# Kernel optimization log

Hardware: AMD Instinct MI355X
Metric: run time of the kernel (lower is better)

## Reference

```python
import jax, jax.numpy as jnp
import numpy as np

INPUT_SIZE = 64
HIDDEN_SIZE = 256
NUM_CLASSES = 10
BATCH = 512
SEQ_LEN = 1024


def setup_inputs() -> dict:
    key = jax.random.key(0)
    ks = jax.random.split(key, 6)
    std = 1.0 / np.sqrt(HIDDEN_SIZE)
    x = jax.random.normal(ks[0], (BATCH, SEQ_LEN, INPUT_SIZE), dtype=jnp.float32)
    # GRUCell params (reset_parameters: uniform(-std, std))
    Wx = jax.random.uniform(ks[1], (3 * HIDDEN_SIZE, INPUT_SIZE), minval=-std, maxval=std, dtype=jnp.float32)
    Wh = jax.random.uniform(ks[2], (3 * HIDDEN_SIZE, HIDDEN_SIZE), minval=-std, maxval=std, dtype=jnp.float32)
    bias = jax.random.uniform(ks[3], (3 * HIDDEN_SIZE,), minval=-std, maxval=std, dtype=jnp.float32)
    # fc: Linear(hidden_size, num_classes), default torch init ~ uniform(-1/sqrt(H), 1/sqrt(H))
    fc_w = jax.random.uniform(ks[4], (NUM_CLASSES, HIDDEN_SIZE), minval=-std, maxval=std, dtype=jnp.float32)
    fc_b = jax.random.uniform(ks[5], (NUM_CLASSES,), minval=-std, maxval=std, dtype=jnp.float32)
    return {"x": x, "Wx": Wx, "Wh": Wh, "bias": bias, "fc_w": fc_w, "fc_b": fc_b}


def reference(x, Wx, Wh, bias, fc_w, fc_b):
    B, S, _ = x.shape
    H = Wh.shape[1]
    b_r, b_z, b_h = jnp.split(bias, 3)
    # Precompute input gates for all timesteps in one GEMM: [B, S, 3H]
    gate_x = jnp.einsum('bsi,gi->bsg', x, Wx)

    def step(h, gx_t):
        gate_h = h @ Wh.T  # [B, 3H]
        i_r, i_z, i_h = jnp.split(gx_t, 3, axis=1)
        h_r, h_z, h_h = jnp.split(gate_h, 3, axis=1)
        reset_gate = jax.nn.sigmoid(i_r + h_r + b_r)
        update_gate = jax.nn.sigmoid(i_z + h_z + b_z)
        new_gate = jnp.tanh(i_h + reset_gate * h_h + b_h)
        hy = new_gate + update_gate * (h - new_gate)
        return hy, None

    h0 = jnp.zeros((B, H), dtype=x.dtype)
    hT, _ = jax.lax.scan(step, h0, jnp.swapaxes(gate_x, 0, 1))  # scan over time
    logit = hT @ fc_w.T + fc_b
    return logit
```

## Files before the change

kernel.cpp:

```cpp
#include <hip/hip_runtime.h>


typedef short v8s __attribute__((ext_vector_type(8)));
typedef float f32x4 __attribute__((ext_vector_type(4)));

#define LOG2E 1.4426950408889634f

__device__ __forceinline__ unsigned short f2b(float f) {
    unsigned int u = __float_as_uint(f);
    u += 0x7FFFu + ((u >> 16) & 1u);
    return (unsigned short)(u >> 16);
}
__device__ __forceinline__ float b2f(unsigned short h) {
    return __uint_as_float(((unsigned int)h) << 16);
}
__device__ __forceinline__ v8s cvt8(f32x4 a, f32x4 b) {
    v8s r;
#pragma unroll
    for (int j = 0; j < 4; ++j) { r[j] = (short)f2b(a[j]); r[4 + j] = (short)f2b(b[j]); }
    return r;
}
__device__ __forceinline__ v8s wfrag(const float* src, float s) {
    f32x4 a = *(const f32x4*)src, b = *(const f32x4*)(src + 4);
    a *= s; b *= s;
    return cvt8(a, b);
}
__device__ __forceinline__ float rcpf(float v) {
#if __has_builtin(__builtin_amdgcn_rcpf)
    return __builtin_amdgcn_rcpf(v);
#else
    return 1.0f / v;
#endif
}
__device__ __forceinline__ float exp2f_(float v) {
#if __has_builtin(__builtin_amdgcn_exp2f)
    return __builtin_amdgcn_exp2f(v);
#else
    return __exp2f(v);
#endif
}
__device__ __forceinline__ float sg(float v) { return rcpf(1.0f + exp2f_(-v)); }
__device__ __forceinline__ f32x4 MF(v8s a, v8s b, f32x4 c) {
    return __builtin_amdgcn_mfma_f32_16x16x32_bf16(a, b, c, 0, 0, 0);
}
__device__ __forceinline__ int fidx(int row, int k) {
    return ((k >> 5) << 9) + ((((k >> 3) & 3) << 4) + row) * 8 + (k & 7);
}

#define LDS_H    131072
#define LDS_X    147456
#define LDS_SIZE 151552

extern "C" __global__ void __launch_bounds__(512, 2)
gru_v7(const float* __restrict__ x, const float* __restrict__ Wx,
       const float* __restrict__ Wh, const float* __restrict__ bias,
       const float* __restrict__ fcw, const float* __restrict__ fcb,
       float* __restrict__ out)
{
    extern __shared__ char lds[];
    v8s* whn = (v8s*)lds;
    char* hl = lds + LDS_H;
    char* xl = lds + LDS_X;

    const int tid = threadIdx.x;
    const int w = tid >> 6, l = tid & 63;
    const int cl = l & 15, kg = l >> 4;
    const int b0 = blockIdx.x << 4;
    const int tiles[6] = {2*w, 2*w+1, 16+2*w, 17+2*w, 32+2*w, 33+2*w};

    for (int f = w; f < 128; f += 8) {
        int t5 = f >> 3, ks = f & 7;
        const float* src = Wh + (size_t)(512 + t5*16 + cl)*256 + ks*32 + kg*8;
        whn[f*64 + l] = wfrag(src, 2.0f*LOG2E);
    }
    v8s whB[4][8];
#pragma unroll
    for (int tt = 0; tt < 4; ++tt) {
        const float* src = Wh + (size_t)(tiles[tt]*16 + cl)*256 + kg*8;
#pragma unroll
        for (int ks = 0; ks < 8; ++ks)
            whB[tt][ks] = wfrag(src + ks*32, LOG2E);
    }
    v8s wxr[12];
#pragma unroll
    for (int tt = 0; tt < 6; ++tt) {
        const float sc = (tt < 4) ? LOG2E : 2.0f*LOG2E;
        const float* s0 = Wx + (size_t)(tiles[tt]*16 + cl)*64 + kg*8;
        wxr[tt*2]   = wfrag(s0, sc);
        wxr[tt*2+1] = wfrag(s0 + 32, sc);
    }
    float brv[2], bzv[2], bhv[2];
#pragma unroll
    for (int p = 0; p < 2; ++p) {
        int ch = (w << 5) + (p << 4) + cl;
        brv[p] = bias[ch] * LOG2E;
        bzv[p] = bias[256 + ch] * LOG2E;
        bhv[p] = bias[512 + ch] * 2.0f*LOG2E;
    }

    for (int i = tid; i < 2048; i += 512) ((unsigned int*)hl)[i] = 0u;
    float hprev[8] = {0, 0, 0, 0, 0, 0, 0, 0};

    const int xr = tid >> 5, xc = (tid & 31) << 1;
    const int xidx = fidx(xr, xc);
    const float* xp = x + (((size_t)(b0 + xr)) << 16) + xc;
    {
        unsigned int pk = (unsigned int)f2b(xp[0]) | ((unsigned int)f2b(xp[1]) << 16);
        *(unsigned int*)(xl + xidx*2) = pk;
    }
    xp += 64;
    const int wn0 = (2*w)*8, wn1 = (2*w+1)*8;

    for (int t = 0; t < 1024; ++t) {
        __syncthreads();
        const int cur = t & 1;
        const v8s* hb = (const v8s*)(hl + cur*8192);
        const v8s* xb = (const v8s*)(xl + cur*2048);

        float xv0 = 0.0f, xv1 = 0.0f;
        if (t < 1023) { xv0 = xp[0]; xv1 = xp[1]; xp += 64; }

        f32x4 acc[8];
        acc[0] = f32x4{brv[0], brv[0], brv[0], brv[0]};
        acc[1] = f32x4{brv[1], brv[1], brv[1], brv[1]};
        acc[2] = f32x4{bzv[0], bzv[0], bzv[0], bzv[0]};
        acc[3] = f32x4{bzv[1], bzv[1], bzv[1], bzv[1]};
        acc[4] = f32x4{0, 0, 0, 0};
        acc[5] = f32x4{0, 0, 0, 0};
        acc[6] = f32x4{bhv[0], bhv[0], bhv[0], bhv[0]};
        acc[7] = f32x4{bhv[1], bhv[1], bhv[1], bhv[1]};

#pragma unroll
        for (int ks = 0; ks < 8; ++ks) {
            v8s a  = hb[(ks << 6) + l];
            v8s n0 = whn[(wn0 + ks)*64 + l];
            v8s n1 = whn[(wn1 + ks)*64 + l];
            acc[0] = MF(a, whB[0][ks], acc[0]);
            acc[1] = MF(a, whB[1][ks], acc[1]);
            acc[2] = MF(a, whB[2][ks], acc[2]);
            acc[3] = MF(a, whB[3][ks], acc[3]);
            acc[4] = MF(a, n0, acc[4]);
            acc[5] = MF(a, n1, acc[5]);
        }
#pragma unroll
        for (int k2 = 0; k2 < 2; ++k2) {
            v8s ax = xb[(k2 << 6) + l];
            acc[0] = MF(ax, wxr[0  + k2], acc[0]);
            acc[1] = MF(ax, wxr[2  + k2], acc[1]);
            acc[2] = MF(ax, wxr[4  + k2], acc[2]);
            acc[3] = MF(ax, wxr[6  + k2], acc[3]);
            acc[6] = MF(ax, wxr[8  + k2], acc[6]);
            acc[7] = MF(ax, wxr[10 + k2], acc[7]);
        }

        unsigned short* hn = (unsigned short*)(hl + (cur ^ 1) * 8192);
#pragma unroll
        for (int p = 0; p < 2; ++p) {
            const int ch = (w << 5) + (p << 4) + cl;
            const int chbase = ((ch >> 5) << 9) + (((ch >> 3) & 3) << 7) + (ch & 7);
#pragma unroll
            for (int i = 0; i < 4; ++i) {
                float rg = sg(acc[p][i]);
                float zg = sg(acc[2 + p][i]);
                float nv = __builtin_fmaf(rg, acc[4 + p][i], acc[6 + p][i]);
                float ng = __builtin_fmaf(2.0f, sg(nv), -1.0f);
                float hy = ng + zg * (hprev[p*4 + i] - ng);
                hprev[p*4 + i] = hy;
                hn[chbase + ((kg << 2) + i) * 8] = f2b(hy);
            }
        }
        if (t < 1023) {
            unsigned int pk = (unsigned int)f2b(xv0) | ((unsigned int)f2b(xv1) << 16);
            *(unsigned int*)(xl + ((cur ^ 1) * 2048) + xidx*2) = pk;
        }
    }

    __syncthreads();
    const unsigned short* hf = (const unsigned short*)hl;
    if (tid < 160) {
        int row = tid / 10, cls = tid - row * 10;
        float s = fcb[cls];
        const float* wrow = fcw + cls * 256;
        for (int k = 0; k < 256; ++k)
            s += b2f(hf[fidx(row, k)]) * wrow[k];
        out[(b0 + row)*10 + cls] = s;
    }
}

extern "C" void kernel_launch(void* const* d_in, const int* in_sizes, int n_in,
                              void* d_out, int out_size, void* d_ws, size_t ws_size,
                              hipStream_t stream) {
    const float* x    = (const float*)d_in[0];
    const float* Wx   = (const float*)d_in[1];
    const float* Wh   = (const float*)d_in[2];
    const float* bias = (const float*)d_in[3];
    const float* fcw  = (const float*)d_in[4];
    const float* fcb  = (const float*)d_in[5];
    (void)d_ws; (void)ws_size;

    (void)hipFuncSetAttribute((const void*)gru_v7,
                              hipFuncAttributeMaxDynamicSharedMemorySize, LDS_SIZE);
    gru_v7<<<dim3(32), dim3(512), LDS_SIZE, stream>>>(
        x, Wx, Wh, bias, fcw, fcb, (float*)d_out);
}
```

Measured before the change: 1.967 ms.

## Double threads per block so each wave owns one 16-channel tile per gate

Raises the block from 512 to 1024 threads (16 waves), so each wave computes one 16-channel tile per gate instead of two. This halves the per-wave MFMA chain and gate math on the serial recurrence critical path. Register-resident weight fragments per thread drop accordingly. In exchange the per-step __syncthreads spans twice as many waves, and each thread now loads one x value rather than two.

Measured after the change: 1.995 ms. No clear change (+1.4%).

```diff
diff --git a/kernel.cpp b/kernel.cpp
--- a/kernel.cpp
+++ b/kernel.cpp
@@ -47,132 +47,105 @@
     return ((k >> 5) << 9) + ((((k >> 3) & 3) << 4) + row) * 8 + (k & 7);
 }
 
-#define LDS_H    131072
-#define LDS_X    147456
-#define LDS_SIZE 151552
+#define LDSX_WN   0
+#define LDSX_H    131072
+#define LDSX_X    147456
+#define LDSX_SIZE 151552
 
-extern "C" __global__ void __launch_bounds__(512, 2)
-gru_v7(const float* __restrict__ x, const float* __restrict__ Wx,
-       const float* __restrict__ Wh, const float* __restrict__ bias,
-       const float* __restrict__ fcw, const float* __restrict__ fcb,
-       float* __restrict__ out)
+extern "C" __global__ void __launch_bounds__(1024, 4)
+gru_v10(const float* __restrict__ x, const float* __restrict__ Wx,
+        const float* __restrict__ Wh, const float* __restrict__ bias,
+        const float* __restrict__ fcw, const float* __restrict__ fcb,
+        float* __restrict__ out)
 {
     extern __shared__ char lds[];
-    v8s* whn = (v8s*)lds;
-    char* hl = lds + LDS_H;
-    char* xl = lds + LDS_X;
+    v8s* wnl = (v8s*)(lds + LDSX_WN);
+    char* hl = lds + LDSX_H;
+    char* xl = lds + LDSX_X;
 
     const int tid = threadIdx.x;
     const int w = tid >> 6, l = tid & 63;
     const int cl = l & 15, kg = l >> 4;
     const int b0 = blockIdx.x << 4;
-    const int tiles[6] = {2*w, 2*w+1, 16+2*w, 17+2*w, 32+2*w, 33+2*w};
+    const int ch = (w << 4) + cl;
 
-    for (int f = w; f < 128; f += 8) {
-        int t5 = f >> 3, ks = f & 7;
-        const float* src = Wh + (size_t)(512 + t5*16 + cl)*256 + ks*32 + kg*8;
-        whn[f*64 + l] = wfrag(src, 2.0f*LOG2E);
+#pragma unroll
+    for (int ks = 0; ks < 8; ++ks)
+        wnl[(w*8 + ks)*64 + l] =
+            wfrag(Wh + (size_t)(512 + ch)*256 + ks*32 + kg*8, 2.0f*LOG2E);
+
+    v8s rW[10], zW[10], nX[2];
+#pragma unroll
+    for (int ks = 0; ks < 8; ++ks) {
+        rW[ks] = wfrag(Wh + (size_t)ch*256 + ks*32 + kg*8, LOG2E);
+        zW[ks] = wfrag(Wh + (size_t)(256 + ch)*256 + ks*32 + kg*8, LOG2E);
     }
-    v8s whB[4][8];
 #pragma unroll
-    for (int tt = 0; tt < 4; ++tt) {
-        const float* src = Wh + (size_t)(tiles[tt]*16 + cl)*256 + kg*8;
-#pragma unroll
-        for (int ks = 0; ks < 8; ++ks)
-            whB[tt][ks] = wfrag(src + ks*32, LOG2E);
+    for (int k2 = 0; k2 < 2; ++k2) {
+        rW[8+k2] = wfrag(Wx + (size_t)ch*64 + k2*32 + kg*8, LOG2E);
+        zW[8+k2] = wfrag(Wx + (size_t)(256 + ch)*64 + k2*32 + kg*8, LOG2E);
+        nX[k2]   = wfrag(Wx + (size_t)(512 + ch)*64 + k2*32 + kg*8, 2.0f*LOG2E);
     }
-    v8s wxr[12];
-#pragma unroll
-    for (int tt = 0; tt < 6; ++tt) {
-        const float sc = (tt < 4) ? LOG2E : 2.0f*LOG2E;
-        const float* s0 = Wx + (size_t)(tiles[tt]*16 + cl)*64 + kg*8;
-        wxr[tt*2]   = wfrag(s0, sc);
-        wxr[tt*2+1] = wfrag(s0 + 32, sc);
+    const float br = bias[ch] * LOG2E;
+    const float bz = bias[256 + ch] * LOG2E;
+    const float bn = bias[512 + ch] * (2.0f*LOG2E);
+
+    const int chb = ((ch >> 5) << 9) + (((ch >> 3) & 3) << 7) + (ch & 7);
+
+    for (int i = tid; i < 2048; i += 1024) ((unsigned int*)hl)[i] = 0u;
+    float hprev[4] = {0, 0, 0, 0};
+
+    const int xr = tid >> 6, xc = tid & 63;
+    const int xidx = fidx(xr, xc);
+    {
+        float v = x[((size_t)(b0 + xr) * 1024 + 0) * 64 + xc];
+        *(unsigned short*)(xl + xidx*2) = f2b(v);
     }
-    float brv[2], bzv[2], bhv[2];
-#pragma unroll
-    for (int p = 0; p < 2; ++p) {
-        int ch = (w << 5) + (p << 4) + cl;
-        brv[p] = bias[ch] * LOG2E;
-        bzv[p] = bias[256 + ch] * LOG2E;
-        bhv[p] = bias[512 + ch] * 2.0f*LOG2E;
-    }
-
-    for (int i = tid; i < 2048; i += 512) ((unsigned int*)hl)[i] = 0u;
-    float hprev[8] = {0, 0, 0, 0, 0, 0, 0, 0};
-
-    const int xr = tid >> 5, xc = (tid & 31) << 1;
-    const int xidx = fidx(xr, xc);
-    const float* xp = x + (((size_t)(b0 + xr)) << 16) + xc;
-    {
-        unsigned int pk = (unsigned int)f2b(xp[0]) | ((unsigned int)f2b(xp[1]) << 16);
-        *(unsigned int*)(xl + xidx*2) = pk;
-    }
-    xp += 64;
-    const int wn0 = (2*w)*8, wn1 = (2*w+1)*8;
 
     for (int t = 0; t < 1024; ++t) {
         __syncthreads();
         const int cur = t & 1;
-        const v8s* hb = (const v8s*)(hl + cur*8192);
-        const v8s* xb = (const v8s*)(xl + cur*2048);
+        const v8s* hb = (const v8s*)(hl + cur * 8192);
+        const v8s* xb = (const v8s*)(xl + cur * 2048);
 
-        float xv0 = 0.0f, xv1 = 0.0f;
-        if (t < 1023) { xv0 = xp[0]; xv1 = xp[1]; xp += 64; }
+        float xv = 0.0f;
+        if (t < 1023)
+            xv = x[((size_t)(b0 + xr) * 1024 + (t + 1)) * 64 + xc];
 
-        f32x4 acc[8];
-        acc[0] = f32x4{brv[0], brv[0], brv[0], brv[0]};
-        acc[1] = f32x4{brv[1], brv[1], brv[1], brv[1]};
-        acc[2] = f32x4{bzv[0], bzv[0], bzv[0], bzv[0]};
-        acc[3] = f32x4{bzv[1], bzv[1], bzv[1], bzv[1]};
-        acc[4] = f32x4{0, 0, 0, 0};
-        acc[5] = f32x4{0, 0, 0, 0};
-        acc[6] = f32x4{bhv[0], bhv[0], bhv[0], bhv[0]};
-        acc[7] = f32x4{bhv[1], bhv[1], bhv[1], bhv[1]};
+        f32x4 aR = {br, br, br, br};
+        f32x4 aZ = {bz, bz, bz, bz};
+        f32x4 aNh = {0, 0, 0, 0};
+        f32x4 aNx = {bn, bn, bn, bn};
 
 #pragma unroll
         for (int ks = 0; ks < 8; ++ks) {
             v8s a  = hb[(ks << 6) + l];
-            v8s n0 = whn[(wn0 + ks)*64 + l];
-            v8s n1 = whn[(wn1 + ks)*64 + l];
-            acc[0] = MF(a, whB[0][ks], acc[0]);
-            acc[1] = MF(a, whB[1][ks], acc[1]);
-            acc[2] = MF(a, whB[2][ks], acc[2]);
-            acc[3] = MF(a, whB[3][ks], acc[3]);
-            acc[4] = MF(a, n0, acc[4]);
-            acc[5] = MF(a, n1, acc[5]);
+            v8s nW = wnl[(w*8 + ks)*64 + l];
+            aR  = MF(a, rW[ks], aR);
+            aZ  = MF(a, zW[ks], aZ);
+            aNh = MF(a, nW, aNh);
         }
 #pragma unroll
         for (int k2 = 0; k2 < 2; ++k2) {
             v8s ax = xb[(k2 << 6) + l];
-            acc[0] = MF(ax, wxr[0  + k2], acc[0]);
-            acc[1] = MF(ax, wxr[2  + k2], acc[1]);
-            acc[2] = MF(ax, wxr[4  + k2], acc[2]);
-            acc[3] = MF(ax, wxr[6  + k2], acc[3]);
-            acc[6] = MF(ax, wxr[8  + k2], acc[6]);
-            acc[7] = MF(ax, wxr[10 + k2], acc[7]);
+            aR  = MF(ax, rW[8+k2], aR);
+            aZ  = MF(ax, zW[8+k2], aZ);
+            aNx = MF(ax, nX[k2], aNx);
         }
 
         unsigned short* hn = (unsigned short*)(hl + (cur ^ 1) * 8192);
 #pragma unroll
-        for (int p = 0; p < 2; ++p) {
-            const int ch = (w << 5) + (p << 4) + cl;
-            const int chbase = ((ch >> 5) << 9) + (((ch >> 3) & 3) << 7) + (ch & 7);
-#pragma unroll
-            for (int i = 0; i < 4; ++i) {
-                float rg = sg(acc[p][i]);
-                float zg = sg(acc[2 + p][i]);
-                float nv = __builtin_fmaf(rg, acc[4 + p][i], acc[6 + p][i]);
-                float ng = __builtin_fmaf(2.0f, sg(nv), -1.0f);
-                float hy = ng + zg * (hprev[p*4 + i] - ng);
-                hprev[p*4 + i] = hy;
-                hn[chbase + ((kg << 2) + i) * 8] = f2b(hy);
-            }
+        for (int i = 0; i < 4; ++i) {
+            float rg = sg(aR[i]);
+            float zg = sg(aZ[i]);
+            float nv = __builtin_fmaf(rg, aNh[i], aNx[i]);
+            float ng = __builtin_fmaf(2.0f, sg(nv), -1.0f);
+            float hy = ng + zg * (hprev[i] - ng);
+            hprev[i] = hy;
+            hn[chb + ((kg << 2) + i) * 8] = f2b(hy);
         }
-        if (t < 1023) {
-            unsigned int pk = (unsigned int)f2b(xv0) | ((unsigned int)f2b(xv1) << 16);
-            *(unsigned int*)(xl + ((cur ^ 1) * 2048) + xidx*2) = pk;
-        }
+        if (t < 1023)
+            *(unsigned short*)(xl + (cur ^ 1) * 2048 + xidx*2) = f2b(xv);
     }
 
     __syncthreads();
@@ -183,7 +156,7 @@
         const float* wrow = fcw + cls * 256;
         for (int k = 0; k < 256; ++k)
             s += b2f(hf[fidx(row, k)]) * wrow[k];
-        out[(b0 + row)*10 + cls] = s;
+        out[(b0 + row) * 10 + cls] = s;
     }
 }
 
@@ -198,8 +171,8 @@
     const float* fcb  = (const float*)d_in[5];
     (void)d_ws; (void)ws_size;
 
-    (void)hipFuncSetAttribute((const void*)gru_v7,
-                              hipFuncAttributeMaxDynamicSharedMemorySize, LDS_SIZE);
-    gru_v7<<<dim3(32), dim3(512), LDS_SIZE, stream>>>(
+    (void)hipFuncSetAttribute((const void*)gru_v10,
+                              hipFuncAttributeMaxDynamicSharedMemorySize, LDSX_SIZE);
+    gru_v10<<<dim3(32), dim3(1024), LDSX_SIZE, stream>>>(
         x, Wx, Wh, bias, fcw, fcb, (float*)d_out);
 }
```

## Split input-gate GEMM into producer blocks streaming fp16 gates via workspace ring

Applied to the files above, without the earlier changes.

Adds a persistent kernel in which 224 producer blocks compute the input-projection gates (x·Wx + bias) in chunks, write them to a global workspace ring buffer as fp16, and signal per-chunk completion through atomic counters. The 32 recurrent blocks spin-wait on these counters and read precomputed gates, so their per-step work is reduced to the h·Wh MFMAs. All of Wh, including the n-gate weights previously held in LDS, now lives in registers, which shrinks the LDS footprint. The design relies on all 256 blocks being co-resident for the spin-wait handshake to make progress, adds global-memory traffic for the gate tensor, and introduces fp16 rounding of the input gates. The old kernel is kept as a fallback when the workspace is too small.

Result: slower. 3.451 ms (+75.5%).

```diff
diff --git a/kernel.cpp b/kernel.cpp
--- a/kernel.cpp
+++ b/kernel.cpp
@@ -1,8 +1,10 @@
 #include <hip/hip_runtime.h>
+#include <hip/hip_fp16.h>
 
 
 typedef short v8s __attribute__((ext_vector_type(8)));
 typedef float f32x4 __attribute__((ext_vector_type(4)));
+typedef unsigned int u32x4 __attribute__((ext_vector_type(4)));
 
 #define LOG2E 1.4426950408889634f
 
@@ -13,6 +15,13 @@
 }
 __device__ __forceinline__ float b2f(unsigned short h) {
     return __uint_as_float(((unsigned int)h) << 16);
+}
+__device__ __forceinline__ unsigned short f2h(float f) {
+    return __half_as_ushort(__float2half_rn(f));
+}
+__device__ __forceinline__ float hxu(unsigned int u, int hi) {
+    unsigned short b = (unsigned short)(hi ? (u >> 16) : (u & 0xFFFFu));
+    return __half2float(__ushort_as_half(b));
 }
 __device__ __forceinline__ v8s cvt8(f32x4 a, f32x4 b) {
     v8s r;
@@ -47,9 +56,197 @@
     return ((k >> 5) << 9) + ((((k >> 3) & 3) << 4) + row) * 8 + (k & 7);
 }
 
-#define LDS_H    131072
-#define LDS_X    147456
-#define LDS_SIZE 151552
+#define LDS11_SIZE 98304
+
+extern "C" __global__ void __launch_bounds__(512, 2)
+gru_v11(const float* __restrict__ x, const float* __restrict__ Wx,
+        const float* __restrict__ Wh, const float* __restrict__ bias,
+        const float* __restrict__ fcw, const float* __restrict__ fcb,
+        unsigned short* __restrict__ gx, unsigned int* __restrict__ ctrl,
+        int n_slots, int cs, float* __restrict__ out)
+{
+    extern __shared__ char lds[];
+    const int tid = threadIdx.x;
+    const int w = tid >> 6, l = tid & 63;
+    const int cl = l & 15, kg = l >> 4;
+    const size_t slot_elems = 393216ull << cs;
+    const int T = 1 << cs;
+    const int tiles[6] = {2*w, 2*w+1, 16+2*w, 17+2*w, 32+2*w, 33+2*w};
+
+    if (blockIdx.x >= 32) {
+        v8s* wxf = (v8s*)lds;
+        const int pid = blockIdx.x - 32;
+        const int cs4 = cs - 4;
+
+        for (int fid = w; fid < 96; fid += 8) {
+            int ct = fid >> 1, k2 = fid & 1;
+            float sc = (ct < 32) ? LOG2E : 2.0f * LOG2E;
+            const float* src = Wx + (size_t)(ct * 16 + cl) * 64 + k2 * 32 + kg * 8;
+            wxf[fid * 64 + l] = wfrag(src, sc);
+        }
+        float bv[6];
+#pragma unroll
+        for (int tt = 0; tt < 6; ++tt)
+            bv[tt] = bias[tiles[tt] * 16 + cl] * ((tt < 4) ? LOG2E : 2.0f * LOG2E);
+        __syncthreads();
+
+        for (int j = pid; j < 2048; j += 224) {
+            const int tc = j >> 5, g = j & 31;
+            const int c = tc >> cs4;
+            const int b0 = g << 4;
+            if (c >= n_slots) {
+                if (tid == 0) {
+                    while (__hip_atomic_load(&ctrl[64 + (c - n_slots)],
+                                             __ATOMIC_ACQUIRE,
+                                             __HIP_MEMORY_SCOPE_AGENT) < 32u)
+                        __builtin_amdgcn_s_sleep(16);
+                }
+                __syncthreads();
+            }
+            unsigned short* gxs = gx + (size_t)(c % n_slots) * slot_elems;
+            const int tl0 = (tc << 4) - (c << cs);
+
+            for (int t16 = 0; t16 < 16; ++t16) {
+                const int t = (tc << 4) + t16;
+                const int tl = tl0 + t16;
+                const float* xs = x + ((size_t)(b0 + cl) * 1024 + t) * 64 + kg * 8;
+                v8s a0 = cvt8(*(const f32x4*)xs,        *(const f32x4*)(xs + 4));
+                v8s a1 = cvt8(*(const f32x4*)(xs + 32), *(const f32x4*)(xs + 36));
+
+                f32x4 acc[6];
+#pragma unroll
+                for (int tt = 0; tt < 6; ++tt)
+                    acc[tt] = f32x4{bv[tt], bv[tt], bv[tt], bv[tt]};
+#pragma unroll
+                for (int tt = 0; tt < 6; ++tt) {
+                    acc[tt] = MF(a0, wxf[(tiles[tt] * 2) * 64 + l], acc[tt]);
+                    acc[tt] = MF(a1, wxf[(tiles[tt] * 2 + 1) * 64 + l], acc[tt]);
+                }
+                unsigned int q[12];
+#pragma unroll
+                for (int tt = 0; tt < 6; ++tt) {
+                    q[tt*2]   = (unsigned int)f2h(acc[tt][0]) | ((unsigned int)f2h(acc[tt][1]) << 16);
+                    q[tt*2+1] = (unsigned int)f2h(acc[tt][2]) | ((unsigned int)f2h(acc[tt][3]) << 16);
+                }
+                unsigned int* gp = (unsigned int*)
+                    (gxs + ((size_t)((g << cs) + tl)) * 12288 + (size_t)tid * 24);
+                u32x4 s0 = {q[0], q[1], q[2],  q[3]};
+                u32x4 s1 = {q[4], q[5], q[6],  q[7]};
+                u32x4 s2 = {q[8], q[9], q[10], q[11]};
+                *(u32x4*)(gp)     = s0;
+                *(u32x4*)(gp + 4) = s1;
+                *(u32x4*)(gp + 8) = s2;
+            }
+            __syncthreads();
+            if (tid == 0)
+                __hip_atomic_fetch_add(&ctrl[c], 1u, __ATOMIC_RELEASE,
+                                       __HIP_MEMORY_SCOPE_AGENT);
+        }
+        return;
+    }
+
+    char* hl = lds;
+    const int g = blockIdx.x;
+    const int b0 = g << 4;
+
+    v8s whB[6][8];
+#pragma unroll
+    for (int tt = 0; tt < 6; ++tt) {
+        const float sc = (tt < 4) ? LOG2E : 2.0f * LOG2E;
+        const float* src = Wh + (size_t)(tiles[tt] * 16 + cl) * 256 + kg * 8;
+#pragma unroll
+        for (int ks = 0; ks < 8; ++ks)
+            whB[tt][ks] = wfrag(src + ks * 32, sc);
+    }
+    float brv[2], bzv[2];
+#pragma unroll
+    for (int p = 0; p < 2; ++p) {
+        const int ch = (w << 5) + (p << 4) + cl;
+        brv[p] = bias[ch] * LOG2E;
+        bzv[p] = bias[256 + ch] * LOG2E;
+    }
+
+    for (int i = tid; i < 2048; i += 512) ((unsigned int*)hl)[i] = 0u;
+    float hprev[8] = {0, 0, 0, 0, 0, 0, 0, 0};
+
+    const unsigned jobs_pc = 32u << (cs - 4);
+    const int nch = 1024 >> cs;
+    int t = 0;
+    for (int c = 0; c < nch; ++c) {
+        if (tid == 0) {
+            while (__hip_atomic_load(&ctrl[c], __ATOMIC_ACQUIRE,
+                                     __HIP_MEMORY_SCOPE_AGENT) < jobs_pc)
+                __builtin_amdgcn_s_sleep(16);
+        }
+        const unsigned short* gq0 = gx + (size_t)(c % n_slots) * slot_elems
+                                   + ((size_t)(g << cs)) * 12288 + (size_t)tid * 24;
+
+        for (int tl = 0; tl < T; ++tl, ++t) {
+            __syncthreads();
+            const int cur = t & 1;
+            const v8s* hb = (const v8s*)(hl + cur * 8192);
+
+            const u32x4* gq = (const u32x4*)(gq0 + (size_t)tl * 12288);
+            u32x4 gr = gq[0], gz = gq[1], gn = gq[2];
+
+            f32x4 aR[2], aZ[2], aN[2];
+            aR[0] = f32x4{brv[0], brv[0], brv[0], brv[0]};
+            aR[1] = f32x4{brv[1], brv[1], brv[1], brv[1]};
+            aZ[0] = f32x4{bzv[0], bzv[0], bzv[0], bzv[0]};
+            aZ[1] = f32x4{bzv[1], bzv[1], bzv[1], bzv[1]};
+            aN[0] = f32x4{0, 0, 0, 0};
+            aN[1] = f32x4{0, 0, 0, 0};
+
+#pragma unroll
+            for (int ks = 0; ks < 8; ++ks) {
+                v8s a = hb[(ks << 6) + l];
+                aR[0] = MF(a, whB[0][ks], aR[0]);
+                aR[1] = MF(a, whB[1][ks], aR[1]);
+                aZ[0] = MF(a, whB[2][ks], aZ[0]);
+                aZ[1] = MF(a, whB[3][ks], aZ[1]);
+                aN[0] = MF(a, whB[4][ks], aN[0]);
+                aN[1] = MF(a, whB[5][ks], aN[1]);
+            }
+
+            unsigned short* hn = (unsigned short*)(hl + (cur ^ 1) * 8192);
+#pragma unroll
+            for (int p = 0; p < 2; ++p) {
+                const int ch = (w << 5) + (p << 4) + cl;
+                const int chbase = ((ch >> 5) << 9) + (((ch >> 3) & 3) << 7) + (ch & 7);
+#pragma unroll
+                for (int i = 0; i < 4; ++i) {
+                    const int dw = p * 2 + (i >> 1), hi = i & 1;
+                    float rg = sg(aR[p][i] + hxu(gr[dw], hi));
+                    float zg = sg(aZ[p][i] + hxu(gz[dw], hi));
+                    float nv = __builtin_fmaf(rg, aN[p][i], hxu(gn[dw], hi));
+                    float ng = __builtin_fmaf(2.0f, sg(nv), -1.0f);
+                    float hy = ng + zg * (hprev[p * 4 + i] - ng);
+                    hprev[p * 4 + i] = hy;
+                    hn[chbase + ((kg << 2) + i) * 8] = f2b(hy);
+                }
+            }
+        }
+        __syncthreads();
+        if (tid == 0)
+            __hip_atomic_fetch_add(&ctrl[64 + c], 1u, __ATOMIC_RELEASE,
+                                   __HIP_MEMORY_SCOPE_AGENT);
+    }
+
+    __syncthreads();
+    const unsigned short* hf = (const unsigned short*)hl;
+    if (tid < 160) {
+        int row = tid / 10, cls = tid - row * 10;
+        float s = fcb[cls];
+        const float* wrow = fcw + cls * 256;
+        for (int k = 0; k < 256; ++k)
+            s += b2f(hf[fidx(row, k)]) * wrow[k];
+        out[(b0 + row) * 10 + cls] = s;
+    }
+}
+
+#define LDS7_H    131072
+#define LDS7_X    147456
+#define LDS7_SIZE 151552
 
 extern "C" __global__ void __launch_bounds__(512, 2)
 gru_v7(const float* __restrict__ x, const float* __restrict__ Wx,
@@ -59,8 +256,8 @@
 {
     extern __shared__ char lds[];
     v8s* whn = (v8s*)lds;
-    char* hl = lds + LDS_H;
-    char* xl = lds + LDS_X;
+    char* hl = lds + LDS7_H;
+    char* xl = lds + LDS7_X;
 
     const int tid = threadIdx.x;
     const int w = tid >> 6, l = tid & 63;
@@ -97,10 +294,8 @@
         bzv[p] = bias[256 + ch] * LOG2E;
         bhv[p] = bias[512 + ch] * 2.0f*LOG2E;
     }
-
     for (int i = tid; i < 2048; i += 512) ((unsigned int*)hl)[i] = 0u;
     float hprev[8] = {0, 0, 0, 0, 0, 0, 0, 0};
-
     const int xr = tid >> 5, xc = (tid & 31) << 1;
     const int xidx = fidx(xr, xc);
     const float* xp = x + (((size_t)(b0 + xr)) << 16) + xc;
@@ -116,7 +311,6 @@
         const int cur = t & 1;
         const v8s* hb = (const v8s*)(hl + cur*8192);
         const v8s* xb = (const v8s*)(xl + cur*2048);
-
         float xv0 = 0.0f, xv1 = 0.0f;
         if (t < 1023) { xv0 = xp[0]; xv1 = xp[1]; xp += 64; }
 
@@ -129,7 +323,6 @@
         acc[5] = f32x4{0, 0, 0, 0};
         acc[6] = f32x4{bhv[0], bhv[0], bhv[0], bhv[0]};
         acc[7] = f32x4{bhv[1], bhv[1], bhv[1], bhv[1]};
-
 #pragma unroll
         for (int ks = 0; ks < 8; ++ks) {
             v8s a  = hb[(ks << 6) + l];
@@ -152,7 +345,6 @@
             acc[6] = MF(ax, wxr[8  + k2], acc[6]);
             acc[7] = MF(ax, wxr[10 + k2], acc[7]);
         }
-
         unsigned short* hn = (unsigned short*)(hl + (cur ^ 1) * 8192);
 #pragma unroll
         for (int p = 0; p < 2; ++p) {
@@ -196,10 +388,31 @@
     const float* bias = (const float*)d_in[3];
     const float* fcw  = (const float*)d_in[4];
     const float* fcb  = (const float*)d_in[5];
-    (void)d_ws; (void)ws_size;
-
-    (void)hipFuncSetAttribute((const void*)gru_v7,
-                              hipFuncAttributeMaxDynamicSharedMemorySize, LDS_SIZE);
-    gru_v7<<<dim3(32), dim3(512), LDS_SIZE, stream>>>(
-        x, Wx, Wh, bias, fcw, fcb, (float*)d_out);
-}
+
+    int cs = -1, n_slots = 0;
+    for (int s = 6; s >= 4; --s) {
+        unsigned long long slot = 786432ull << s;
+        if (ws_size < 1024ull + 2ull * slot) continue;
+        int nch = 1024 >> s;
+        unsigned long long n = (ws_size - 1024ull) / slot;
+        n_slots = (n > (unsigned long long)nch) ? nch : (int)n;
+        cs = s;
+        break;
+    }
+
+    if (cs >= 4) {
+        unsigned int* ctrl =
+            (unsigned int*)((char*)d_ws + (786432ull << cs) * (size_t)n_slots);
+        (void)hipMemsetAsync(ctrl, 0, 1024, stream);
+        (void)hipFuncSetAttribute((const void*)gru_v11,
+                                  hipFuncAttributeMaxDynamicSharedMemorySize, LDS11_SIZE);
+        gru_v11<<<dim3(256), dim3(512), LDS11_SIZE, stream>>>(
+            x, Wx, Wh, bias, fcw, fcb,
+            (unsigned short*)d_ws, ctrl, n_slots, cs, (float*)d_out);
+    } else {
+        (void)hipFuncSetAttribute((const void*)gru_v7,
+                                  hipFuncAttributeMaxDynamicSharedMemorySize, LDS7_SIZE);
+        gru_v7<<<dim3(32), dim3(512), LDS7_SIZE, stream>>>(
+            x, Wx, Wh, bias, fcw, fcb, (float*)d_out);
+    }
+}
```
